# Optimization experiments

Hardware: AMD Instinct MI355X
Metric: run time of the kernel (lower is better)

Reference implementation:

```python
import jax, jax.numpy as jnp
import numpy as np

HIDDEN = 256
NUM_NODES = 262144
NUM_GRAPHS = 4096
CHUNK_SIZE = 32  # hard-coded in the torch forward
NUM_CHUNKS = NUM_GRAPHS // CHUNK_SIZE


def setup_inputs() -> dict:
    key = jax.random.key(0)
    k1, k2, k3, k4 = jax.random.split(key, 4)
    x = jax.random.normal(k1, (NUM_NODES, HIDDEN), dtype=jnp.float32)
    # sorted graph ids covering all graphs 0..NUM_GRAPHS-1 (PyG batch vector)
    batch = (jnp.arange(NUM_NODES, dtype=jnp.int64) * NUM_GRAPHS) // NUM_NODES
    # attention MLP params: Linear(H,H) -> Tanh -> Linear(H,1, bias=False)
    s1 = 1.0 / np.sqrt(HIDDEN)
    W1 = jax.random.uniform(k2, (HIDDEN, HIDDEN), jnp.float32, -s1, s1)
    b1 = jax.random.uniform(k3, (HIDDEN,), jnp.float32, -s1, s1)
    W2 = jax.random.uniform(k4, (HIDDEN, 1), jnp.float32, -s1, s1)
    return {"x": x, "batch": batch, "W1": W1, "b1": b1, "W2": W2}


def reference(x, batch, W1, b1, W2):
    # attention scores: Linear -> Tanh -> Linear (no bias)  [N]
    scores = (jnp.tanh(x @ W1 + b1) @ W2)[:, 0]
    # softmax is over ALL nodes within each chunk of 32 consecutive graphs
    chunk_id = batch // CHUNK_SIZE
    m = jax.ops.segment_max(scores, chunk_id, num_segments=NUM_CHUNKS)
    e = jnp.exp(scores - m[chunk_id])
    denom = jax.ops.segment_sum(e, chunk_id, num_segments=NUM_CHUNKS)
    w = e / denom[chunk_id]  # [N]
    # global_add_pool of (w * x) per graph  -> [NUM_GRAPHS, HIDDEN]
    out = jax.ops.segment_sum(w[:, None] * x, batch, num_segments=NUM_GRAPHS)
    return out
```

## Files before the change

### kernel.cpp

```cpp
#include <hip/hip_runtime.h>

#define NODES 262144
#define HID 256
#define GRAPHS 4096
#define ROWS 32
#define TPB 8

typedef __attribute__((ext_vector_type(8))) short short8;
typedef __attribute__((ext_vector_type(4))) short short4v;
typedef __attribute__((ext_vector_type(4))) float floatx4;

__device__ __forceinline__ short bf16_rne(float f) {
  union { float f; unsigned int u; } v; v.f = f;
  unsigned int u = v.u;
  u += 0x7fffu + ((u >> 16) & 1u);
  return (short)(u >> 16);
}

__device__ __forceinline__ float fast_tanh(float x) {
  float e = __expf(2.0f * x);
  return 1.0f - 2.0f * __builtin_amdgcn_rcpf(e + 1.0f);
}

__global__ __launch_bounds__(256) void k_prep(const float* __restrict__ w1,
                                              short* __restrict__ w1t) {
  int k = blockIdx.x, n = threadIdx.x;
  w1t[n * HID + k] = bf16_rne(w1[k * HID + n]);
}

__global__ __launch_bounds__(256) void k_scores(
    const float* __restrict__ x, const short* __restrict__ w1t,
    const float* __restrict__ b1, const float* __restrict__ w2,
    float* __restrict__ scores)
{
  __shared__ short As[ROWS * 264];
  __shared__ float part[4][ROWS];
  const int tid = threadIdx.x;
  const int wave = tid >> 6, lane = tid & 63;
  const int quad = lane >> 4, l15 = lane & 15;

  const short* bbase = w1t + (wave * 64 + l15) * HID + quad * 8;
  const short* abase = &As[l15 * 264 + quad * 8];

  float b1v[4], w2v[4];
#pragma unroll
  for (int ct = 0; ct < 4; ++ct) {
    int n = wave * 64 + ct * 16 + l15;
    b1v[ct] = b1[n];
    w2v[ct] = w2[n];
  }

  const int tile0 = blockIdx.x * TPB;

  float4 r[8];
  {
    const float4* xin = ((const float4*)x) + (size_t)tile0 * (ROWS * 64);
#pragma unroll
    for (int i = 0; i < 8; ++i) r[i] = xin[tid + i * 256];
  }

  for (int tt = 0; tt < TPB; ++tt) {
    __syncthreads();

#pragma unroll
    for (int i = 0; i < 8; ++i) {
      int f = tid + i * 256;
      int row = f >> 6, c4 = f & 63;
      short4v b;
      b.x = bf16_rne(r[i].x); b.y = bf16_rne(r[i].y);
      b.z = bf16_rne(r[i].z); b.w = bf16_rne(r[i].w);
      *(short4v*)&As[row * 264 + c4 * 4] = b;
    }
    __syncthreads();

    if (tt + 1 < TPB) {
      const float4* xin =
          ((const float4*)x) + (size_t)(tile0 + tt + 1) * (ROWS * 64);
#pragma unroll
      for (int i = 0; i < 8; ++i) r[i] = xin[tid + i * 256];
    }

    floatx4 acc[2][4];
#pragma unroll
    for (int rt = 0; rt < 2; ++rt)
#pragma unroll
      for (int ct = 0; ct < 4; ++ct)
#pragma unroll
        for (int e = 0; e < 4; ++e) acc[rt][ct][e] = 0.f;

#pragma unroll
    for (int kk = 0; kk < 8; ++kk) {
      short8 bfrag[4];
#pragma unroll
      for (int ct = 0; ct < 4; ++ct)
        bfrag[ct] = *(const short8*)(bbase + ct * 16 * HID + kk * 32);
      short8 afrag[2];
#pragma unroll
      for (int rt = 0; rt < 2; ++rt)
        afrag[rt] = *(const short8*)(abase + rt * 16 * 264 + kk * 32);
#pragma unroll
      for (int rt = 0; rt < 2; ++rt)
#pragma unroll
        for (int ct = 0; ct < 4; ++ct)
          acc[rt][ct] = __builtin_amdgcn_mfma_f32_16x16x32_bf16(
              afrag[rt], bfrag[ct], acc[rt][ct], 0, 0, 0);
    }

    float sc[2][4];
#pragma unroll
    for (int rt = 0; rt < 2; ++rt)
#pragma unroll
      for (int reg = 0; reg < 4; ++reg) {
        float s = 0.f;
#pragma unroll
        for (int ct = 0; ct < 4; ++ct)
          s += fast_tanh(acc[rt][ct][reg] + b1v[ct]) * w2v[ct];
        sc[rt][reg] = s;
      }
#pragma unroll
    for (int mask = 1; mask <= 8; mask <<= 1)
#pragma unroll
      for (int rt = 0; rt < 2; ++rt)
#pragma unroll
        for (int reg = 0; reg < 4; ++reg)
          sc[rt][reg] += __shfl_xor(sc[rt][reg], mask, 64);
    if (l15 == 0) {
#pragma unroll
      for (int rt = 0; rt < 2; ++rt)
#pragma unroll
        for (int reg = 0; reg < 4; ++reg)
          part[wave][rt * 16 + quad * 4 + reg] = sc[rt][reg];
    }
    __syncthreads();
    if (tid < ROWS)
      scores[(size_t)(tile0 + tt) * ROWS + tid] =
          part[0][tid] + part[1][tid] + part[2][tid] + part[3][tid];
  }
}

__global__ __launch_bounds__(256) void k_stats(const float* __restrict__ scores,
                                               float* __restrict__ mout,
                                               float* __restrict__ dout) {
  int c = blockIdx.x, t = threadIdx.x;
  const float4* s4 = ((const float4*)scores) + (size_t)c * 512;
  float4 a = s4[t * 2], b = s4[t * 2 + 1];
  float mx = fmaxf(fmaxf(fmaxf(a.x, a.y), fmaxf(a.z, a.w)),
                   fmaxf(fmaxf(b.x, b.y), fmaxf(b.z, b.w)));
#pragma unroll
  for (int mask = 1; mask < 64; mask <<= 1)
    mx = fmaxf(mx, __shfl_xor(mx, mask, 64));
  __shared__ float redm[4], reds[4];
  int wave = t >> 6, lane = t & 63;
  if (lane == 0) redm[wave] = mx;
  __syncthreads();
  mx = fmaxf(fmaxf(redm[0], redm[1]), fmaxf(redm[2], redm[3]));
  float s = expf(a.x - mx) + expf(a.y - mx) + expf(a.z - mx) + expf(a.w - mx) +
            expf(b.x - mx) + expf(b.y - mx) + expf(b.z - mx) + expf(b.w - mx);
#pragma unroll
  for (int mask = 1; mask < 64; mask <<= 1)
    s += __shfl_xor(s, mask, 64);
  if (lane == 0) reds[wave] = s;
  __syncthreads();
  if (t == 0) {
    mout[c] = mx;
    dout[c] = reds[0] + reds[1] + reds[2] + reds[3];
  }
}

__global__ __launch_bounds__(256) void k_pool(const float* __restrict__ x,
                                              const float* __restrict__ scores,
                                              const float* __restrict__ mbuf,
                                              const float* __restrict__ dbuf,
                                              float* __restrict__ out) {
  const int wave = threadIdx.x >> 6, lane = threadIdx.x & 63;
  const int g = blockIdx.x * 4 + wave;
  const int c = g >> 5;
  float s = scores[(size_t)g * 64 + lane];
  float w = __expf(s - mbuf[c]) / dbuf[c];

  const float4* xb = (const float4*)(x + (size_t)g * 64 * HID);
  float4 acc = make_float4(0.f, 0.f, 0.f, 0.f);
#pragma unroll 16
  for (int i = 0; i < 64; ++i) {
    float wi = __shfl(w, i, 64);
    float4 v = xb[i * 64 + lane];
    acc.x = fmaf(wi, v.x, acc.x);
    acc.y = fmaf(wi, v.y, acc.y);
    acc.z = fmaf(wi, v.z, acc.z);
    acc.w = fmaf(wi, v.w, acc.w);
  }
  ((float4*)out)[(size_t)g * 64 + lane] = acc;
}

extern "C" void kernel_launch(void* const* d_in, const int* in_sizes, int n_in,
                              void* d_out, int out_size, void* d_ws, size_t ws_size,
                              hipStream_t stream) {
  const float* x  = (const float*)d_in[0];
  const float* w1 = (const float*)d_in[2];
  const float* b1 = (const float*)d_in[3];
  const float* w2 = (const float*)d_in[4];
  float* out = (float*)d_out;

  char* ws = (char*)d_ws;
  float* scores = (float*)ws;
  float* mbuf   = (float*)(ws + (1 << 20));
  float* dbuf   = mbuf + 128;
  short* w1t    = (short*)(ws + (1 << 20) + 4096);

  k_prep  <<<256, 256, 0, stream>>>(w1, w1t);
  k_scores<<<NODES / (ROWS * TPB), 256, 0, stream>>>(x, w1t, b1, w2, scores);
  k_stats <<<128, 256, 0, stream>>>(scores, mbuf, dbuf);
  k_pool  <<<GRAPHS / 4, 256, 0, stream>>>(x, scores, mbuf, dbuf, out);
}
```

Measured before the change: 421.5 us.

## Fuse softmax-weighted pooling into scoring kernel with per-tile online softmax partials

The scoring kernel now computes a per-32-row local max and exp-sum, then accumulates exp-weighted partial sums of the tile's rows straight from the LDS copy. A small finish kernel rescales and combines these partials per chunk and per graph. This removes the separate stats kernel and the second full read of x in the pooling kernel. In exchange, the pooled sum uses the bf16-rounded x held in LDS rather than the fp32 input, which lowers output precision.

```diff
diff --git a/kernel.cpp b/kernel.cpp
--- a/kernel.cpp
+++ b/kernel.cpp
@@ -5,6 +5,7 @@
 #define GRAPHS 4096
 #define ROWS 32
 #define TPB 8
+#define NHALF (NODES / ROWS)
 
 typedef __attribute__((ext_vector_type(8))) short short8;
 typedef __attribute__((ext_vector_type(4))) short short4v;
@@ -17,6 +18,12 @@
   return (short)(u >> 16);
 }
 
+__device__ __forceinline__ float bf16_to_f32(unsigned short u) {
+  union { unsigned int u; float f; } v;
+  v.u = ((unsigned int)u) << 16;
+  return v.f;
+}
+
 __device__ __forceinline__ float fast_tanh(float x) {
   float e = __expf(2.0f * x);
   return 1.0f - 2.0f * __builtin_amdgcn_rcpf(e + 1.0f);
@@ -28,13 +35,14 @@
   w1t[n * HID + k] = bf16_rne(w1[k * HID + n]);
 }
 
-__global__ __launch_bounds__(256) void k_scores(
+__global__ __launch_bounds__(256) void k_fused(
     const float* __restrict__ x, const short* __restrict__ w1t,
     const float* __restrict__ b1, const float* __restrict__ w2,
-    float* __restrict__ scores)
+    float* __restrict__ Ah, float* __restrict__ mh, float* __restrict__ lh)
 {
   __shared__ short As[ROWS * 264];
   __shared__ float part[4][ROWS];
+  __shared__ float wbuf[ROWS];
   const int tid = threadIdx.x;
   const int wave = tid >> 6, lane = tid & 63;
   const int quad = lane >> 4, l15 = lane & 15;
@@ -50,11 +58,11 @@
     w2v[ct] = w2[n];
   }
 
-  const int tile0 = blockIdx.x * TPB;
+  const int half0 = blockIdx.x * TPB;
 
   float4 r[8];
   {
-    const float4* xin = ((const float4*)x) + (size_t)tile0 * (ROWS * 64);
+    const float4* xin = ((const float4*)x) + (size_t)half0 * (ROWS * 64);
 #pragma unroll
     for (int i = 0; i < 8; ++i) r[i] = xin[tid + i * 256];
   }
@@ -75,7 +83,7 @@
 
     if (tt + 1 < TPB) {
       const float4* xin =
-          ((const float4*)x) + (size_t)(tile0 + tt + 1) * (ROWS * 64);
+          ((const float4*)x) + (size_t)(half0 + tt + 1) * (ROWS * 64);
 #pragma unroll
       for (int i = 0; i < 8; ++i) r[i] = xin[tid + i * 256];
     }
@@ -132,64 +140,58 @@
           part[wave][rt * 16 + quad * 4 + reg] = sc[rt][reg];
     }
     __syncthreads();
-    if (tid < ROWS)
-      scores[(size_t)(tile0 + tt) * ROWS + tid] =
-          part[0][tid] + part[1][tid] + part[2][tid] + part[3][tid];
-  }
-}
-
-__global__ __launch_bounds__(256) void k_stats(const float* __restrict__ scores,
-                                               float* __restrict__ mout,
-                                               float* __restrict__ dout) {
-  int c = blockIdx.x, t = threadIdx.x;
-  const float4* s4 = ((const float4*)scores) + (size_t)c * 512;
-  float4 a = s4[t * 2], b = s4[t * 2 + 1];
-  float mx = fmaxf(fmaxf(fmaxf(a.x, a.y), fmaxf(a.z, a.w)),
-                   fmaxf(fmaxf(b.x, b.y), fmaxf(b.z, b.w)));
-#pragma unroll
-  for (int mask = 1; mask < 64; mask <<= 1)
-    mx = fmaxf(mx, __shfl_xor(mx, mask, 64));
-  __shared__ float redm[4], reds[4];
-  int wave = t >> 6, lane = t & 63;
-  if (lane == 0) redm[wave] = mx;
+
+    if (tid < ROWS) {
+      float s = part[0][tid] + part[1][tid] + part[2][tid] + part[3][tid];
+      float m = s;
+#pragma unroll
+      for (int mask = 1; mask < 32; mask <<= 1)
+        m = fmaxf(m, __shfl_xor(m, mask, 32));
+      float e = __expf(s - m);
+      float l = e;
+#pragma unroll
+      for (int mask = 1; mask < 32; mask <<= 1)
+        l += __shfl_xor(l, mask, 32);
+      wbuf[tid] = e;
+      if (tid == 0) { mh[half0 + tt] = m; lh[half0 + tt] = l; }
+    }
+    __syncthreads();
+
+    float pacc = 0.f;
+#pragma unroll
+    for (int i = 0; i < ROWS; ++i) {
+      float w = wbuf[i];
+      unsigned short u = *(const unsigned short*)&As[i * 264 + tid];
+      pacc = fmaf(w, bf16_to_f32(u), pacc);
+    }
+    Ah[(size_t)(half0 + tt) * HID + tid] = pacc;
+  }
+}
+
+__global__ __launch_bounds__(256) void k_finish(
+    const float* __restrict__ Ah, const float* __restrict__ mh,
+    const float* __restrict__ lh, float* __restrict__ out)
+{
+  const int c = blockIdx.x, t = threadIdx.x;
+  __shared__ float sm[64], sl[64], sh[64];
+  if (t < 64) { sm[t] = mh[c * 64 + t]; sl[t] = lh[c * 64 + t]; }
   __syncthreads();
-  mx = fmaxf(fmaxf(redm[0], redm[1]), fmaxf(redm[2], redm[3]));
-  float s = expf(a.x - mx) + expf(a.y - mx) + expf(a.z - mx) + expf(a.w - mx) +
-            expf(b.x - mx) + expf(b.y - mx) + expf(b.z - mx) + expf(b.w - mx);
-#pragma unroll
-  for (int mask = 1; mask < 64; mask <<= 1)
-    s += __shfl_xor(s, mask, 64);
-  if (lane == 0) reds[wave] = s;
+  float m = sm[0];
+#pragma unroll 8
+  for (int j = 1; j < 64; ++j) m = fmaxf(m, sm[j]);
+  float den = 0.f;
+#pragma unroll 8
+  for (int j = 0; j < 64; ++j) den += sl[j] * __expf(sm[j] - m);
+  float inv = 1.0f / den;
+  if (t < 64) sh[t] = __expf(sm[t] - m) * inv;
   __syncthreads();
-  if (t == 0) {
-    mout[c] = mx;
-    dout[c] = reds[0] + reds[1] + reds[2] + reds[3];
-  }
-}
-
-__global__ __launch_bounds__(256) void k_pool(const float* __restrict__ x,
-                                              const float* __restrict__ scores,
-                                              const float* __restrict__ mbuf,
-                                              const float* __restrict__ dbuf,
-                                              float* __restrict__ out) {
-  const int wave = threadIdx.x >> 6, lane = threadIdx.x & 63;
-  const int g = blockIdx.x * 4 + wave;
-  const int c = g >> 5;
-  float s = scores[(size_t)g * 64 + lane];
-  float w = __expf(s - mbuf[c]) / dbuf[c];
-
-  const float4* xb = (const float4*)(x + (size_t)g * 64 * HID);
-  float4 acc = make_float4(0.f, 0.f, 0.f, 0.f);
-#pragma unroll 16
-  for (int i = 0; i < 64; ++i) {
-    float wi = __shfl(w, i, 64);
-    float4 v = xb[i * 64 + lane];
-    acc.x = fmaf(wi, v.x, acc.x);
-    acc.y = fmaf(wi, v.y, acc.y);
-    acc.z = fmaf(wi, v.z, acc.z);
-    acc.w = fmaf(wi, v.w, acc.w);
-  }
-  ((float4*)out)[(size_t)g * 64 + lane] = acc;
+  const float* ab = Ah + (size_t)c * 64 * HID;
+#pragma unroll 4
+  for (int j = 0; j < 32; ++j) {
+    float v = ab[(2 * j) * HID + t] * sh[2 * j] +
+              ab[(2 * j + 1) * HID + t] * sh[2 * j + 1];
+    out[((size_t)c * 32 + j) * HID + t] = v;
+  }
 }
 
 extern "C" void kernel_launch(void* const* d_in, const int* in_sizes, int n_in,
@@ -202,13 +204,12 @@
   float* out = (float*)d_out;
 
   char* ws = (char*)d_ws;
-  float* scores = (float*)ws;
-  float* mbuf   = (float*)(ws + (1 << 20));
-  float* dbuf   = mbuf + 128;
-  short* w1t    = (short*)(ws + (1 << 20) + 4096);
+  float* Ah  = (float*)ws;
+  float* mhb = (float*)(ws + (NHALF * HID) * 4);
+  float* lhb = mhb + NHALF;
+  short* w1t = (short*)(ws + (NHALF * HID + 2 * NHALF) * 4);
 
   k_prep  <<<256, 256, 0, stream>>>(w1, w1t);
-  k_scores<<<NODES / (ROWS * TPB), 256, 0, stream>>>(x, w1t, b1, w2, scores);
-  k_stats <<<128, 256, 0, stream>>>(scores, mbuf, dbuf);
-  k_pool  <<<GRAPHS / 4, 256, 0, stream>>>(x, scores, mbuf, dbuf, out);
-}
+  k_fused <<<NODES / (ROWS * TPB), 256, 0, stream>>>(x, w1t, b1, w2, Ah, mhb, lhb);
+  k_finish<<<GRAPHS / 32, 256, 0, stream>>>(Ah, mhb, lhb, out);
+}
```

After: 391.0 us. 7.2% less time.
